# Kernel tuning notes

Hardware: AMD Instinct MI355X
Metric: run time of the kernel (lower is better)

The kernel has to match this reference:

```python
import jax, jax.numpy as jnp
import numpy as np

EPS_NORM = 1e-12  # F.normalize eps
EPS_BN = 1e-5     # BatchNorm1d eps


def _gather_neighbors(tensor, index):
    # tensor: (bs, v, d), index: (bs, v, n) -> (bs, v, n, d)
    return jax.vmap(lambda t, i: t[i])(tensor, index)


def setup_inputs() -> dict:
    key = jax.random.key(0)
    ks = jax.random.split(key, 8)
    bs, v, n = 4, 4096, 32
    cin, cout = 128, 256
    stdv = float(np.sqrt(2.0 / cout))
    return {
        "neighbor_index": jax.random.randint(ks[0], (bs, v, n), 0, v),
        "vertices": jax.random.normal(ks[1], (bs, v, 3), dtype=jnp.float32),
        "feature_map": jax.random.normal(ks[2], (bs, v, cin - 1), dtype=jnp.float32),
        "directions": jax.random.uniform(ks[3], (4, cout), minval=-stdv, maxval=stdv, dtype=jnp.float32),
        "W": jax.random.normal(ks[4], (cout, cin), dtype=jnp.float32) / np.sqrt(cin),
        "b": jnp.zeros((cout,), jnp.float32),
        "gamma": jnp.ones((cout,), jnp.float32),
        "beta": jnp.zeros((cout,), jnp.float32),
    }


def reference(neighbor_index, vertices, feature_map, directions, W, b, gamma, beta):
    # --- direction-based weights theta: (bs, v, n, cout) ---
    neighbors = _gather_neighbors(vertices, neighbor_index)          # (bs,v,n,3)
    direc = neighbors - vertices[:, :, None, :]
    direc_norm = direc / jnp.maximum(
        jnp.linalg.norm(direc, axis=-1, keepdims=True), EPS_NORM)    # F.normalize
    dir_w = (direc_norm + 1.0) * 0.5                                  # (bs,v,n,3)
    sup_w = jnp.stack([directions[1] - directions[0],
                       directions[2] - directions[0],
                       directions[3] - directions[0]], axis=0)        # (3, cout)
    theta = jax.nn.relu(jnp.einsum('bvnk,kc->bvnc', dir_w, sup_w) + directions[0])

    # --- gathered features + L2 distance channel ---
    fs = _gather_neighbors(feature_map, neighbor_index)               # (bs,v,n,cin-1)
    fdist = jnp.sqrt(jnp.sum(fs * fs, axis=-1, keepdims=True))        # (bs,v,n,1)
    fs = jnp.concatenate([fs, fdist], axis=-1)                        # (bs,v,n,cin)

    # --- Linear -> BatchNorm1d (training stats) -> ReLU ---
    z = jnp.einsum('bvni,ci->bvnc', fs, W) + b                        # (bs,v,n,cout)
    mean = jnp.mean(z, axis=(0, 1, 2))
    var = jnp.mean(jnp.square(z - mean), axis=(0, 1, 2))              # biased var
    zn = (z - mean) * jax.lax.rsqrt(var + EPS_BN) * gamma + beta
    act = jax.nn.relu(zn) * theta

    # --- max-pool over neighbor dim ---
    return jnp.max(act, axis=2)                                       # (bs,v,cout)
```

## Files before the change

### kernel.cpp

```cpp
#include <hip/hip_runtime.h>

typedef unsigned short ushort_t;
typedef __attribute__((ext_vector_type(8))) short short8;
typedef __attribute__((ext_vector_type(4))) float floatx4;
typedef __attribute__((ext_vector_type(2))) float floatx2;

#define NN    32
#define CIN   128
#define COUT  256
#define NPTS  16384
#define NSAMP (NPTS * NN)
#define LDA   136
#define HB    128

__device__ __align__(16) ushort_t g_wb[COUT * CIN];
__device__ __align__(16) ushort_t g_y[(size_t)NPTS * COUT];
__device__ __align__(16) int      g_hp[HB * 4096];
__device__ __align__(16) float    g_sp[256 * 512];
__device__ __align__(16) float    g_consts[1536];

__device__ __forceinline__ float bf2f(ushort_t u) {
    return __uint_as_float(((unsigned int)u) << 16);
}
__device__ __forceinline__ ushort_t f2bf(float f) {
    unsigned int x = __float_as_uint(f);
    return (ushort_t)((x + 0x7FFFu + ((x >> 16) & 1u)) >> 16);
}
__device__ __forceinline__ int probe_f32(const void* verts, int lane) {
    float ax = fabsf(bf2f(((const ushort_t*)verts)[lane]));
    unsigned long long b = __ballot((ax > 1e-5f) && (ax < 32.0f));
    return (__popcll(b) >= 56) ? 0 : 1;
}

__global__ __launch_bounds__(256)
void hist_kernel(const int* __restrict__ nbr,
                 const void* __restrict__ Wg,
                 const void* __restrict__ verts) {
    __shared__ int h[4096];
    const int b   = blockIdx.x;
    const int tid = threadIdx.x;
    if (b < HB) {
        #pragma unroll
        for (int i = 0; i < 16; ++i) h[i * 256 + tid] = 0;
        __syncthreads();
        const int* src = nbr + (size_t)b * 4096;
        #pragma unroll
        for (int i = 0; i < 16; ++i) atomicAdd(&h[src[i * 256 + tid]], 1);
        __syncthreads();
        int* dst = g_hp + (size_t)b * 4096;
        #pragma unroll
        for (int i = 0; i < 16; ++i) dst[i * 256 + tid] = h[i * 256 + tid];
    } else {
        const int f32 = probe_f32(verts, tid & 63);
        int i = (b - HB) * 1024 + tid * 4;
        if (f32) {
            float4 v = ((const float4*)Wg)[i >> 2];
            g_wb[i] = f2bf(v.x); g_wb[i + 1] = f2bf(v.y);
            g_wb[i + 2] = f2bf(v.z); g_wb[i + 3] = f2bf(v.w);
        } else {
            *(uint2*)(g_wb + i) = *(const uint2*)((const ushort_t*)Wg + i);
        }
    }
}

__global__ __launch_bounds__(256, 2)
void ygemm_kernel(const void* __restrict__ fm, const void* __restrict__ verts) {
    __shared__ __align__(16) ushort_t At[64 * LDA];
    __shared__ float multS[64];

    const int tid  = threadIdx.x;
    const int r0   = blockIdx.x * 64;
    const int lane = tid & 63;
    const int f32  = probe_f32(verts, lane);

    if (tid < 64) {
        const int* hp = g_hp + (size_t)(r0 >> 12) * 32 * 4096 + (r0 & 4095) + tid;
        int s = 0;
        #pragma unroll
        for (int p2 = 0; p2 < 32; ++p2) s += hp[(size_t)p2 * 4096];
        multS[tid] = (float)s;
    }

    const int rl4 = tid >> 6;
    #pragma unroll 4
    for (int i = 0; i < 16; ++i) {
        const int rl = i * 4 + rl4;
        float f0, f1; ushort_t u0, u1;
        if (f32) {
            const float* src = (const float*)fm + (size_t)(r0 + rl) * 127;
            f0 = src[lane];
            f1 = (lane < 63) ? src[64 + lane] : 0.0f;
            u0 = f2bf(f0); u1 = f2bf(f1);
        } else {
            const ushort_t* src = (const ushort_t*)fm + (size_t)(r0 + rl) * 127;
            u0 = src[lane];
            u1 = (lane < 63) ? src[64 + lane] : (ushort_t)0;
            f0 = bf2f(u0); f1 = bf2f(u1);
        }
        float ss = f0 * f0 + f1 * f1;
        #pragma unroll
        for (int d = 1; d < 64; d <<= 1) ss += __shfl_xor(ss, d, 64);
        At[rl * LDA + lane]      = u0;
        At[rl * LDA + 64 + lane] = (lane < 63) ? u1 : f2bf(sqrtf(ss));
    }
    __syncthreads();

    const int w = tid >> 6;
    const int m = lane & 15;
    const int q = lane >> 4;

    floatx4 acc[4][4];
    #pragma unroll
    for (int rt = 0; rt < 4; ++rt)
        #pragma unroll
        for (int ct = 0; ct < 4; ++ct)
            acc[rt][ct] = (floatx4){0.0f, 0.0f, 0.0f, 0.0f};

    #pragma unroll
    for (int kk = 0; kk < 4; ++kk) {
        const int kof = kk * 32 + q * 8;
        short8 af[4];
        #pragma unroll
        for (int rt = 0; rt < 4; ++rt)
            af[rt] = *(const short8*)&At[(rt * 16 + m) * LDA + kof];
        short8 bfr[4];
        #pragma unroll
        for (int ct = 0; ct < 4; ++ct) {
            int ch = w * 64 + ct * 16 + m;
            bfr[ct] = *(const short8*)(g_wb + ch * CIN + kof);
        }
        #pragma unroll
        for (int rt = 0; rt < 4; ++rt)
            #pragma unroll
            for (int ct = 0; ct < 4; ++ct)
                acc[rt][ct] = __builtin_amdgcn_mfma_f32_16x16x32_bf16(
                    af[rt], bfr[ct], acc[rt][ct], 0, 0, 0);
    }

    #pragma unroll
    for (int ct = 0; ct < 4; ++ct) {
        const int ch = w * 64 + ct * 16 + m;
        float s = 0.0f, ss = 0.0f;
        #pragma unroll
        for (int rt = 0; rt < 4; ++rt)
            #pragma unroll
            for (int j = 0; j < 4; ++j) {
                int rloc = rt * 16 + q * 4 + j;
                ushort_t yb = f2bf(acc[rt][ct][j]);
                g_y[(size_t)(r0 + rloc) * COUT + ch] = yb;
                float yv = bf2f(yb);
                float wm = multS[rloc];
                s  += wm * yv;
                ss += wm * yv * yv;
            }
        s  += __shfl_xor(s, 16, 64);  s  += __shfl_xor(s, 32, 64);
        ss += __shfl_xor(ss, 16, 64); ss += __shfl_xor(ss, 32, 64);
        if (q == 0) {
            g_sp[(size_t)blockIdx.x * 512 + ch]       = s;
            g_sp[(size_t)blockIdx.x * 512 + 256 + ch] = ss;
        }
    }
}

__global__ void finalize_kernel(const void* __restrict__ gamma,
                                const void* __restrict__ beta,
                                const void* __restrict__ dirs,
                                const void* __restrict__ verts) {
    const int c   = threadIdx.x;
    const int f32 = probe_f32(verts, c & 63);

    float s = 0.0f, ss = 0.0f;
    #pragma unroll 8
    for (int p2 = 0; p2 < 256; ++p2) {
        s  += g_sp[(size_t)p2 * 512 + c];
        ss += g_sp[(size_t)p2 * 512 + 256 + c];
    }
    const float invN = 1.0f / (float)NSAMP;
    float mean = s * invN;
    float var  = fmaxf(ss * invN - mean * mean, 0.0f);
    float inv  = 1.0f / sqrtf(var + 1e-5f);
    float ga, be, d0, d1, d2, d3;
    if (f32) {
        ga = ((const float*)gamma)[c]; be = ((const float*)beta)[c];
        const float* dd = (const float*)dirs;
        d0 = dd[c]; d1 = dd[256 + c]; d2 = dd[512 + c]; d3 = dd[768 + c];
    } else {
        ga = bf2f(((const ushort_t*)gamma)[c]); be = bf2f(((const ushort_t*)beta)[c]);
        const ushort_t* dd = (const ushort_t*)dirs;
        d0 = bf2f(dd[c]); d1 = bf2f(dd[256 + c]);
        d2 = bf2f(dd[512 + c]); d3 = bf2f(dd[768 + c]);
    }
    float scale = ga * inv;
    g_consts[c]        = scale;
    g_consts[256 + c]  = be - mean * scale;
    g_consts[512 + c]  = d0;
    g_consts[768 + c]  = d1 - d0;
    g_consts[1024 + c] = d2 - d0;
    g_consts[1280 + c] = d3 - d0;
}

__global__ __launch_bounds__(128, 4)
void epi_kernel(const int* __restrict__ nbr,
                const void* __restrict__ verts,
                void* __restrict__ out) {
    __shared__ int    rows[NN];
    __shared__ float4 dws[NN];
    __shared__ __align__(16) float cS[1536];
    __shared__ float4 xm1[64];

    const int tid  = threadIdx.x;
    const int bid  = blockIdx.x;
    const int p    = ((bid & 7) << 11) | (bid >> 3);
    const int lane = tid & 63;
    const int f32  = probe_f32(verts, lane);

    #pragma unroll
    for (int k = 0; k < 3; ++k) {
        int i4 = (k * 128 + tid) * 4;
        *(float4*)&cS[i4] = *(const float4*)&g_consts[i4];
    }
    if (tid < NN) {
        int gv = ((p >> 12) << 12) + nbr[p * NN + tid];
        rows[tid] = gv;
        float sx, sy, sz, nx, ny, nz;
        if (f32) {
            const float* vv = (const float*)verts;
            sx = vv[p * 3]; sy = vv[p * 3 + 1]; sz = vv[p * 3 + 2];
            nx = vv[gv * 3]; ny = vv[gv * 3 + 1]; nz = vv[gv * 3 + 2];
        } else {
            const ushort_t* vv = (const ushort_t*)verts;
            sx = bf2f(vv[p * 3]); sy = bf2f(vv[p * 3 + 1]); sz = bf2f(vv[p * 3 + 2]);
            nx = bf2f(vv[gv * 3]); ny = bf2f(vv[gv * 3 + 1]); nz = bf2f(vv[gv * 3 + 2]);
        }
        float dx = nx - sx, dy = ny - sy, dz = nz - sz;
        float nrm = sqrtf(dx * dx + dy * dy + dz * dz);
        float inv = 1.0f / fmaxf(nrm, 1e-12f);
        dws[tid] = make_float4((dx * inv + 1.0f) * 0.5f,
                               (dy * inv + 1.0f) * 0.5f,
                               (dz * inv + 1.0f) * 0.5f, 0.0f);
    }
    __syncthreads();

    const int w  = tid >> 6;
    const int c4 = lane * 4;
    const floatx4 zero = {0.0f, 0.0f, 0.0f, 0.0f};
    const floatx4 sc = *(const floatx4*)&cS[c4];
    const floatx4 sh = *(const floatx4*)&cS[256 + c4];
    const floatx4 d0 = *(const floatx4*)&cS[512 + c4];
    const floatx4 s0 = *(const floatx4*)&cS[768 + c4];
    const floatx4 s1 = *(const floatx4*)&cS[1024 + c4];
    const floatx4 s2 = *(const floatx4*)&cS[1280 + c4];

    floatx4 vm0 = zero, vm1 = zero, vm2 = zero, vm3 = zero;
    #pragma unroll
    for (int j0 = 0; j0 < 16; j0 += 4) {
        #pragma unroll
        for (int jj = 0; jj < 4; ++jj) {
            const int j = w * 16 + j0 + jj;
            int rb = __builtin_amdgcn_readfirstlane(rows[j]);
            const uint2 u = *(const uint2*)(g_y + (size_t)rb * COUT + c4);
            floatx4 y;
            y.x = __uint_as_float(u.x << 16);
            y.y = __uint_as_float(u.x & 0xFFFF0000u);
            y.z = __uint_as_float(u.y << 16);
            y.w = __uint_as_float(u.y & 0xFFFF0000u);
            float4 dw = dws[j];
            floatx4 th = d0 + s0 * dw.x + s1 * dw.y + s2 * dw.z;
            th = __builtin_elementwise_max(th, zero);
            floatx4 zt = (y * sc + sh) * th;
            if      (jj == 0) vm0 = __builtin_elementwise_max(vm0, zt);
            else if (jj == 1) vm1 = __builtin_elementwise_max(vm1, zt);
            else if (jj == 2) vm2 = __builtin_elementwise_max(vm2, zt);
            else              vm3 = __builtin_elementwise_max(vm3, zt);
        }
    }
    floatx4 vm = __builtin_elementwise_max(
        __builtin_elementwise_max(vm0, vm1),
        __builtin_elementwise_max(vm2, vm3));

    if (w == 1) xm1[lane] = make_float4(vm.x, vm.y, vm.z, vm.w);
    __syncthreads();
    if (w == 0) {
        float4 o = xm1[lane];
        vm = __builtin_elementwise_max(vm, (floatx4){o.x, o.y, o.z, o.w});
        size_t ofs = (size_t)p * COUT + c4;
        if (f32) {
            *(floatx4*)((float*)out + ofs) = vm;
        } else {
            uint2 ou;
            ou.x = ((unsigned int)f2bf(vm.y) << 16) | (unsigned int)f2bf(vm.x);
            ou.y = ((unsigned int)f2bf(vm.w) << 16) | (unsigned int)f2bf(vm.z);
            *(uint2*)((ushort_t*)out + ofs) = ou;
        }
    }
}

extern "C" void kernel_launch(void* const* d_in, const int* in_sizes, int n_in,
                              void* d_out, int out_size, void* d_ws, size_t ws_size,
                              hipStream_t stream) {
    const int* nbr    = (const int*)d_in[0];
    const void* verts = d_in[1];
    const void* fm    = d_in[2];
    const void* dirs  = d_in[3];
    const void* Wg    = d_in[4];
    const void* gamma = d_in[6];
    const void* beta  = d_in[7];
    (void)d_ws; (void)ws_size; (void)in_sizes; (void)n_in; (void)out_size;

    hist_kernel<<<dim3(HB + 32), dim3(256), 0, stream>>>(nbr, Wg, verts);
    ygemm_kernel<<<dim3(NPTS / 64), dim3(256), 0, stream>>>(fm, verts);
    finalize_kernel<<<dim3(1), dim3(256), 0, stream>>>(gamma, beta, dirs, verts);
    epi_kernel<<<dim3(NPTS), dim3(128), 0, stream>>>(nbr, verts, d_out);
}
```

Before: 148.5 us.

## Restructure epilogue so each half-wave handles one point over all neighbors

The epilogue kernel now processes 8 points per 256-thread block, with each 32-lane half-wave owning one point and every lane covering 8 channels across all 32 neighbors. This removes the cross-wave max reduction through shared memory and the second barrier. The gathered row index is packed into the direction float4, and the per-channel constants are read straight from global memory instead of being staged in LDS. Loads widen to 16 bytes per lane and there are fewer blocks. In exchange, rows are no longer wave-uniform, so the scalar readfirstlane path is lost, and register pressure rises.

```diff
diff --git a/kernel.cpp b/kernel.cpp
--- a/kernel.cpp
+++ b/kernel.cpp
@@ -199,29 +199,24 @@
     g_consts[1280 + c] = d3 - d0;
 }
 
-__global__ __launch_bounds__(128, 4)
+__global__ __launch_bounds__(256, 4)
 void epi_kernel(const int* __restrict__ nbr,
                 const void* __restrict__ verts,
                 void* __restrict__ out) {
-    __shared__ int    rows[NN];
-    __shared__ float4 dws[NN];
-    __shared__ __align__(16) float cS[1536];
-    __shared__ float4 xm1[64];
+    __shared__ float4 dws[8][NN];
 
     const int tid  = threadIdx.x;
+    const int w    = tid >> 6;
+    const int lane = tid & 63;
+    const int h    = lane >> 5;
+    const int j    = lane & 31;
     const int bid  = blockIdx.x;
-    const int p    = ((bid & 7) << 11) | (bid >> 3);
-    const int lane = tid & 63;
+    const int p0   = (((bid & 7) << 8) | (bid >> 3)) << 3;
+    const int p    = p0 + 2 * w + h;
     const int f32  = probe_f32(verts, lane);
 
-    #pragma unroll
-    for (int k = 0; k < 3; ++k) {
-        int i4 = (k * 128 + tid) * 4;
-        *(float4*)&cS[i4] = *(const float4*)&g_consts[i4];
-    }
-    if (tid < NN) {
-        int gv = ((p >> 12) << 12) + nbr[p * NN + tid];
-        rows[tid] = gv;
+    {
+        int gv = ((p >> 12) << 12) + nbr[(size_t)p * NN + j];
         float sx, sy, sz, nx, ny, nz;
         if (f32) {
             const float* vv = (const float*)verts;
@@ -235,63 +230,79 @@
         float dx = nx - sx, dy = ny - sy, dz = nz - sz;
         float nrm = sqrtf(dx * dx + dy * dy + dz * dz);
         float inv = 1.0f / fmaxf(nrm, 1e-12f);
-        dws[tid] = make_float4((dx * inv + 1.0f) * 0.5f,
-                               (dy * inv + 1.0f) * 0.5f,
-                               (dz * inv + 1.0f) * 0.5f, 0.0f);
+        dws[2 * w + h][j] = make_float4((dx * inv + 1.0f) * 0.5f,
+                                        (dy * inv + 1.0f) * 0.5f,
+                                        (dz * inv + 1.0f) * 0.5f,
+                                        __int_as_float(gv));
     }
     __syncthreads();
 
-    const int w  = tid >> 6;
-    const int c4 = lane * 4;
+    const int cb = (lane & 31) * 8;
     const floatx4 zero = {0.0f, 0.0f, 0.0f, 0.0f};
-    const floatx4 sc = *(const floatx4*)&cS[c4];
-    const floatx4 sh = *(const floatx4*)&cS[256 + c4];
-    const floatx4 d0 = *(const floatx4*)&cS[512 + c4];
-    const floatx4 s0 = *(const floatx4*)&cS[768 + c4];
-    const floatx4 s1 = *(const floatx4*)&cS[1024 + c4];
-    const floatx4 s2 = *(const floatx4*)&cS[1280 + c4];
-
-    floatx4 vm0 = zero, vm1 = zero, vm2 = zero, vm3 = zero;
-    #pragma unroll
-    for (int j0 = 0; j0 < 16; j0 += 4) {
+    const floatx4 scL = *(const floatx4*)&g_consts[cb];
+    const floatx4 scH = *(const floatx4*)&g_consts[cb + 4];
+    const floatx4 shL = *(const floatx4*)&g_consts[256 + cb];
+    const floatx4 shH = *(const floatx4*)&g_consts[256 + cb + 4];
+    const floatx4 d0L = *(const floatx4*)&g_consts[512 + cb];
+    const floatx4 d0H = *(const floatx4*)&g_consts[512 + cb + 4];
+    const floatx4 s0L = *(const floatx4*)&g_consts[768 + cb];
+    const floatx4 s0H = *(const floatx4*)&g_consts[768 + cb + 4];
+    const floatx4 s1L = *(const floatx4*)&g_consts[1024 + cb];
+    const floatx4 s1H = *(const floatx4*)&g_consts[1024 + cb + 4];
+    const floatx4 s2L = *(const floatx4*)&g_consts[1280 + cb];
+    const floatx4 s2H = *(const floatx4*)&g_consts[1280 + cb + 4];
+
+    const float4* dwp = dws[2 * w + h];
+    floatx4 vmL0 = zero, vmH0 = zero, vmL1 = zero, vmH1 = zero;
+
+    for (int j0 = 0; j0 < NN; j0 += 4) {
+        float4 dw[4]; uint4 u[4];
         #pragma unroll
         for (int jj = 0; jj < 4; ++jj) {
-            const int j = w * 16 + j0 + jj;
-            int rb = __builtin_amdgcn_readfirstlane(rows[j]);
-            const uint2 u = *(const uint2*)(g_y + (size_t)rb * COUT + c4);
-            floatx4 y;
-            y.x = __uint_as_float(u.x << 16);
-            y.y = __uint_as_float(u.x & 0xFFFF0000u);
-            y.z = __uint_as_float(u.y << 16);
-            y.w = __uint_as_float(u.y & 0xFFFF0000u);
-            float4 dw = dws[j];
-            floatx4 th = d0 + s0 * dw.x + s1 * dw.y + s2 * dw.z;
-            th = __builtin_elementwise_max(th, zero);
-            floatx4 zt = (y * sc + sh) * th;
-            if      (jj == 0) vm0 = __builtin_elementwise_max(vm0, zt);
-            else if (jj == 1) vm1 = __builtin_elementwise_max(vm1, zt);
-            else if (jj == 2) vm2 = __builtin_elementwise_max(vm2, zt);
-            else              vm3 = __builtin_elementwise_max(vm3, zt);
-        }
-    }
-    floatx4 vm = __builtin_elementwise_max(
-        __builtin_elementwise_max(vm0, vm1),
-        __builtin_elementwise_max(vm2, vm3));
-
-    if (w == 1) xm1[lane] = make_float4(vm.x, vm.y, vm.z, vm.w);
-    __syncthreads();
-    if (w == 0) {
-        float4 o = xm1[lane];
-        vm = __builtin_elementwise_max(vm, (floatx4){o.x, o.y, o.z, o.w});
-        size_t ofs = (size_t)p * COUT + c4;
-        if (f32) {
-            *(floatx4*)((float*)out + ofs) = vm;
-        } else {
-            uint2 ou;
-            ou.x = ((unsigned int)f2bf(vm.y) << 16) | (unsigned int)f2bf(vm.x);
-            ou.y = ((unsigned int)f2bf(vm.w) << 16) | (unsigned int)f2bf(vm.z);
-            *(uint2*)((ushort_t*)out + ofs) = ou;
-        }
+            dw[jj] = dwp[j0 + jj];
+            int row = __float_as_int(dw[jj].w);
+            u[jj] = *(const uint4*)(g_y + ((size_t)row << 8) + cb);
+        }
+        #pragma unroll
+        for (int jj = 0; jj < 4; ++jj) {
+            floatx4 yL, yH;
+            yL.x = __uint_as_float(u[jj].x << 16);
+            yL.y = __uint_as_float(u[jj].x & 0xFFFF0000u);
+            yL.z = __uint_as_float(u[jj].y << 16);
+            yL.w = __uint_as_float(u[jj].y & 0xFFFF0000u);
+            yH.x = __uint_as_float(u[jj].z << 16);
+            yH.y = __uint_as_float(u[jj].z & 0xFFFF0000u);
+            yH.z = __uint_as_float(u[jj].w << 16);
+            yH.w = __uint_as_float(u[jj].w & 0xFFFF0000u);
+            floatx4 thL = d0L + s0L * dw[jj].x + s1L * dw[jj].y + s2L * dw[jj].z;
+            floatx4 thH = d0H + s0H * dw[jj].x + s1H * dw[jj].y + s2H * dw[jj].z;
+            thL = __builtin_elementwise_max(thL, zero);
+            thH = __builtin_elementwise_max(thH, zero);
+            floatx4 ztL = (yL * scL + shL) * thL;
+            floatx4 ztH = (yH * scH + shH) * thH;
+            if (jj & 1) {
+                vmL1 = __builtin_elementwise_max(vmL1, ztL);
+                vmH1 = __builtin_elementwise_max(vmH1, ztH);
+            } else {
+                vmL0 = __builtin_elementwise_max(vmL0, ztL);
+                vmH0 = __builtin_elementwise_max(vmH0, ztH);
+            }
+        }
+    }
+    floatx4 vmL = __builtin_elementwise_max(vmL0, vmL1);
+    floatx4 vmH = __builtin_elementwise_max(vmH0, vmH1);
+
+    size_t ofs = (size_t)p * COUT + cb;
+    if (f32) {
+        *(floatx4*)((float*)out + ofs)     = vmL;
+        *(floatx4*)((float*)out + ofs + 4) = vmH;
+    } else {
+        uint4 ou;
+        ou.x = ((unsigned int)f2bf(vmL.y) << 16) | (unsigned int)f2bf(vmL.x);
+        ou.y = ((unsigned int)f2bf(vmL.w) << 16) | (unsigned int)f2bf(vmL.z);
+        ou.z = ((unsigned int)f2bf(vmH.y) << 16) | (unsigned int)f2bf(vmH.x);
+        ou.w = ((unsigned int)f2bf(vmH.w) << 16) | (unsigned int)f2bf(vmH.z);
+        *(uint4*)((ushort_t*)out + ofs) = ou;
     }
 }
 
@@ -310,5 +321,5 @@
     hist_kernel<<<dim3(HB + 32), dim3(256), 0, stream>>>(nbr, Wg, verts);
     ygemm_kernel<<<dim3(NPTS / 64), dim3(256), 0, stream>>>(fm, verts);
     finalize_kernel<<<dim3(1), dim3(256), 0, stream>>>(gamma, beta, dirs, verts);
-    epi_kernel<<<dim3(NPTS), dim3(128), 0, stream>>>(nbr, verts, d_out);
-}
+    epi_kernel<<<dim3(NPTS / 8), dim3(256), 0, stream>>>(nbr, verts, d_out);
+}
```

Result: faster. 139.1 us (-6.3%).

## Process four points per epilogue block, one wave per point

Applied to the files above, without the earlier changes.

The epilogue kernel now handles four points per 256-thread block, with each wave covering all 32 neighbors of one point. This removes the cross-wave max reduction and its second barrier. The gathered row index is packed into the w slot of the direction float4 in shared memory. Constants are read straight from global memory instead of being staged through LDS. Neighbor loads are batched four at a time to expose memory-level parallelism, at the cost of a longer serial loop per wave and a block remap that changes the locality of point ordering.

```diff
diff --git a/kernel.cpp b/kernel.cpp
--- a/kernel.cpp
+++ b/kernel.cpp
@@ -199,29 +199,22 @@
     g_consts[1280 + c] = d3 - d0;
 }
 
-__global__ __launch_bounds__(128, 4)
+__global__ __launch_bounds__(256, 4)
 void epi_kernel(const int* __restrict__ nbr,
                 const void* __restrict__ verts,
                 void* __restrict__ out) {
-    __shared__ int    rows[NN];
-    __shared__ float4 dws[NN];
-    __shared__ __align__(16) float cS[1536];
-    __shared__ float4 xm1[64];
+    __shared__ float4 dws[4][NN];
 
     const int tid  = threadIdx.x;
+    const int lane = tid & 63;
     const int bid  = blockIdx.x;
-    const int p    = ((bid & 7) << 11) | (bid >> 3);
-    const int lane = tid & 63;
+    const int p0   = (((bid & 7) << 9) | (bid >> 3)) << 2;
     const int f32  = probe_f32(verts, lane);
 
-    #pragma unroll
-    for (int k = 0; k < 3; ++k) {
-        int i4 = (k * 128 + tid) * 4;
-        *(float4*)&cS[i4] = *(const float4*)&g_consts[i4];
-    }
-    if (tid < NN) {
-        int gv = ((p >> 12) << 12) + nbr[p * NN + tid];
-        rows[tid] = gv;
+    if (tid < 128) {
+        const int pt = tid >> 5, j = tid & 31;
+        const int p  = p0 + pt;
+        int gv = ((p >> 12) << 12) + nbr[(size_t)p * NN + j];
         float sx, sy, sz, nx, ny, nz;
         if (f32) {
             const float* vv = (const float*)verts;
@@ -235,63 +228,59 @@
         float dx = nx - sx, dy = ny - sy, dz = nz - sz;
         float nrm = sqrtf(dx * dx + dy * dy + dz * dz);
         float inv = 1.0f / fmaxf(nrm, 1e-12f);
-        dws[tid] = make_float4((dx * inv + 1.0f) * 0.5f,
-                               (dy * inv + 1.0f) * 0.5f,
-                               (dz * inv + 1.0f) * 0.5f, 0.0f);
+        dws[pt][j] = make_float4((dx * inv + 1.0f) * 0.5f,
+                                 (dy * inv + 1.0f) * 0.5f,
+                                 (dz * inv + 1.0f) * 0.5f,
+                                 __int_as_float(gv));
     }
     __syncthreads();
 
     const int w  = tid >> 6;
+    const int p  = p0 + w;
     const int c4 = lane * 4;
     const floatx4 zero = {0.0f, 0.0f, 0.0f, 0.0f};
-    const floatx4 sc = *(const floatx4*)&cS[c4];
-    const floatx4 sh = *(const floatx4*)&cS[256 + c4];
-    const floatx4 d0 = *(const floatx4*)&cS[512 + c4];
-    const floatx4 s0 = *(const floatx4*)&cS[768 + c4];
-    const floatx4 s1 = *(const floatx4*)&cS[1024 + c4];
-    const floatx4 s2 = *(const floatx4*)&cS[1280 + c4];
-
-    floatx4 vm0 = zero, vm1 = zero, vm2 = zero, vm3 = zero;
-    #pragma unroll
-    for (int j0 = 0; j0 < 16; j0 += 4) {
+    const floatx4 sc = *(const floatx4*)&g_consts[c4];
+    const floatx4 sh = *(const floatx4*)&g_consts[256 + c4];
+    const floatx4 d0 = *(const floatx4*)&g_consts[512 + c4];
+    const floatx4 s0 = *(const floatx4*)&g_consts[768 + c4];
+    const floatx4 s1 = *(const floatx4*)&g_consts[1024 + c4];
+    const floatx4 s2 = *(const floatx4*)&g_consts[1280 + c4];
+
+    const float4* dwp = dws[w];
+    floatx4 vmA = zero, vmB = zero;
+
+    for (int j0 = 0; j0 < NN; j0 += 4) {
+        float4 dw[4]; uint2 u[4];
         #pragma unroll
         for (int jj = 0; jj < 4; ++jj) {
-            const int j = w * 16 + j0 + jj;
-            int rb = __builtin_amdgcn_readfirstlane(rows[j]);
-            const uint2 u = *(const uint2*)(g_y + (size_t)rb * COUT + c4);
+            dw[jj] = dwp[j0 + jj];
+            int row = __float_as_int(dw[jj].w);
+            u[jj] = *(const uint2*)(g_y + ((size_t)row << 8) + c4);
+        }
+        #pragma unroll
+        for (int jj = 0; jj < 4; ++jj) {
             floatx4 y;
-            y.x = __uint_as_float(u.x << 16);
-            y.y = __uint_as_float(u.x & 0xFFFF0000u);
-            y.z = __uint_as_float(u.y << 16);
-            y.w = __uint_as_float(u.y & 0xFFFF0000u);
-            float4 dw = dws[j];
-            floatx4 th = d0 + s0 * dw.x + s1 * dw.y + s2 * dw.z;
+            y.x = __uint_as_float(u[jj].x << 16);
+            y.y = __uint_as_float(u[jj].x & 0xFFFF0000u);
+            y.z = __uint_as_float(u[jj].y << 16);
+            y.w = __uint_as_float(u[jj].y & 0xFFFF0000u);
+            floatx4 th = d0 + s0 * dw[jj].x + s1 * dw[jj].y + s2 * dw[jj].z;
             th = __builtin_elementwise_max(th, zero);
             floatx4 zt = (y * sc + sh) * th;
-            if      (jj == 0) vm0 = __builtin_elementwise_max(vm0, zt);
-            else if (jj == 1) vm1 = __builtin_elementwise_max(vm1, zt);
-            else if (jj == 2) vm2 = __builtin_elementwise_max(vm2, zt);
-            else              vm3 = __builtin_elementwise_max(vm3, zt);
-        }
-    }
-    floatx4 vm = __builtin_elementwise_max(
-        __builtin_elementwise_max(vm0, vm1),
-        __builtin_elementwise_max(vm2, vm3));
-
-    if (w == 1) xm1[lane] = make_float4(vm.x, vm.y, vm.z, vm.w);
-    __syncthreads();
-    if (w == 0) {
-        float4 o = xm1[lane];
-        vm = __builtin_elementwise_max(vm, (floatx4){o.x, o.y, o.z, o.w});
-        size_t ofs = (size_t)p * COUT + c4;
-        if (f32) {
-            *(floatx4*)((float*)out + ofs) = vm;
-        } else {
-            uint2 ou;
-            ou.x = ((unsigned int)f2bf(vm.y) << 16) | (unsigned int)f2bf(vm.x);
-            ou.y = ((unsigned int)f2bf(vm.w) << 16) | (unsigned int)f2bf(vm.z);
-            *(uint2*)((ushort_t*)out + ofs) = ou;
-        }
+            if (jj & 1) vmB = __builtin_elementwise_max(vmB, zt);
+            else        vmA = __builtin_elementwise_max(vmA, zt);
+        }
+    }
+    floatx4 vm = __builtin_elementwise_max(vmA, vmB);
+
+    size_t ofs = (size_t)p * COUT + c4;
+    if (f32) {
+        *(floatx4*)((float*)out + ofs) = vm;
+    } else {
+        uint2 ou;
+        ou.x = ((unsigned int)f2bf(vm.y) << 16) | (unsigned int)f2bf(vm.x);
+        ou.y = ((unsigned int)f2bf(vm.w) << 16) | (unsigned int)f2bf(vm.z);
+        *(uint2*)((ushort_t*)out + ofs) = ou;
     }
 }
 
@@ -310,5 +299,5 @@
     hist_kernel<<<dim3(HB + 32), dim3(256), 0, stream>>>(nbr, Wg, verts);
     ygemm_kernel<<<dim3(NPTS / 64), dim3(256), 0, stream>>>(fm, verts);
     finalize_kernel<<<dim3(1), dim3(256), 0, stream>>>(gamma, beta, dirs, verts);
-    epi_kernel<<<dim3(NPTS), dim3(128), 0, stream>>>(nbr, verts, d_out);
-}
+    epi_kernel<<<dim3(NPTS / 4), dim3(256), 0, stream>>>(nbr, verts, d_out);
+}
```

After: 141.0 us. -5.1%, faster.
